# Performance work log

Measured on AMD Instinct MI355X. Metric: run time of the kernel, lower is better.

## Reference

```python
import jax, jax.numpy as jnp
import numpy as np

B, S, D = 2, 2048, 4096
N_HEADS, N_KV_HEADS = 32, 8
HEAD_DIM = D // N_HEADS  # 128
N_REP = N_HEADS // N_KV_HEADS
NEG_INF = -1e9  # finite stand-in for -inf additive causal mask


def apply_rotary_emb(x, freqs_cis):
    # x: [b, s, h, hd]; freqs_cis: [s, hd//2, 2] (cos, sin)
    b, s, h, hd = x.shape
    xr = x.reshape(b, s, h, hd // 2, 2)
    fc = freqs_cis.reshape(1, s, 1, hd // 2, 2)
    o0 = xr[..., 0] * fc[..., 0] - xr[..., 1] * fc[..., 1]
    o1 = xr[..., 1] * fc[..., 0] + xr[..., 0] * fc[..., 1]
    return jnp.stack([o0, o1], axis=-1).reshape(b, s, h, hd)


def setup_inputs() -> dict:
    key = jax.random.key(0)
    ks = jax.random.split(key, 6)
    x = jax.random.normal(ks[0], (B, S, D), dtype=jnp.float32)
    # weights stored torch-style: [out_features, in_features]
    wq = jax.random.normal(ks[1], (N_HEADS * HEAD_DIM, D), dtype=jnp.float32) * 0.02
    wk = jax.random.normal(ks[2], (N_KV_HEADS * HEAD_DIM, D), dtype=jnp.float32) * 0.02
    wv = jax.random.normal(ks[3], (N_KV_HEADS * HEAD_DIM, D), dtype=jnp.float32) * 0.02
    wo = jax.random.normal(ks[4], (D, N_HEADS * HEAD_DIM), dtype=jnp.float32) * 0.02
    # rotary table (Llama-style, theta=10000)
    inv_freq = 1.0 / (10000.0 ** (np.arange(0, HEAD_DIM, 2, dtype=np.float32) / HEAD_DIM))
    angles = np.arange(S, dtype=np.float32)[:, None] * inv_freq[None, :]
    freqs_cis = jnp.asarray(np.stack([np.cos(angles), np.sin(angles)], axis=-1))  # [S, hd//2, 2]
    # additive causal mask
    mask = jnp.where(jnp.tril(jnp.ones((S, S), dtype=bool)), 0.0, NEG_INF).astype(jnp.float32)
    return {"x": x, "start_pos": 0, "freqs_cis": freqs_cis, "mask": mask,
            "wq": wq, "wk": wk, "wv": wv, "wo": wo}


def reference(x, start_pos, freqs_cis, mask, wq, wk, wv, wo):
    b, s, _ = x.shape
    xq = jnp.einsum('bsd,ed->bse', x, wq).reshape(b, s, N_HEADS, HEAD_DIM)
    xk = jnp.einsum('bsd,ed->bse', x, wk).reshape(b, s, N_KV_HEADS, HEAD_DIM)
    xv = jnp.einsum('bsd,ed->bse', x, wv).reshape(b, s, N_KV_HEADS, HEAD_DIM)
    xq = apply_rotary_emb(xq, freqs_cis)
    xk = apply_rotary_emb(xk, freqs_cis)
    # repeat_kv (repeat_interleave along head dim)
    xk = jnp.repeat(xk, N_REP, axis=2)
    xv = jnp.repeat(xv, N_REP, axis=2)
    q = xq.transpose(0, 2, 1, 3)  # [b, h, s, hd]
    k = xk.transpose(0, 2, 1, 3)
    v = xv.transpose(0, 2, 1, 3)
    scores = jnp.einsum('bhqd,bhkd->bhqk', q, k) / jnp.sqrt(jnp.float32(HEAD_DIM))
    scores = scores + mask[None, None, :, :]
    probs = jax.nn.softmax(scores.astype(jnp.float32), axis=-1).astype(q.dtype)
    out = jnp.einsum('bhqk,bhkd->bhqd', probs, v)
    out = out.transpose(0, 2, 1, 3).reshape(b, s, N_HEADS * HEAD_DIM)
    return jnp.einsum('bse,de->bsd', out, wo)
```

## Files before the change

### kernel.cpp

```cpp
#include <hip/hip_runtime.h>
#include <cstdint>
#include <cstddef>

#define B_   2
#define S_   2048
#define D_   4096
#define H_   32
#define KVH_ 8
#define HD_  128

typedef unsigned short u16;
typedef short     bf16x8 __attribute__((ext_vector_type(8)));
typedef float     f32x4  __attribute__((ext_vector_type(4)));
typedef float     f32x16 __attribute__((ext_vector_type(16)));
typedef u16       u16x8  __attribute__((ext_vector_type(8)));
typedef uint32_t  u32x2  __attribute__((ext_vector_type(2)));
typedef uint32_t  u32x4  __attribute__((ext_vector_type(4)));

__device__ __forceinline__ u16 f2bf(float f) {
  union { float f; uint32_t u; } v; v.f = f;
  uint32_t u = v.u;
  return (u16)((u + 0x7fffu + ((u >> 16) & 1u)) >> 16);
}
__device__ __forceinline__ float bf2f(u16 h) {
  union { uint32_t u; float f; } v; v.u = ((uint32_t)h) << 16;
  return v.f;
}
__device__ __forceinline__ uint32_t cvtpk(float lo, float hi_) {
  uint32_t r; asm("v_cvt_pk_bf16_f32 %0, %1, %2" : "=v"(r) : "v"(lo), "v"(hi_)); return r;
}
__device__ __forceinline__ float exp2v(float x) {
  float r; asm("v_exp_f32 %0, %1" : "=v"(r) : "v"(x)); return r;
}

__device__ __forceinline__ void gl_lds16(const void* g, void* l) {
  __builtin_amdgcn_global_load_lds(
      (const __attribute__((address_space(1))) void*)g,
      (__attribute__((address_space(3))) void*)l, 16, 0, 0);
}

#define MFMA(a, b, c)  __builtin_amdgcn_mfma_f32_16x16x32_bf16((a), (b), (c), 0, 0, 0)
#define MFMA32(a, b, c) __builtin_amdgcn_mfma_f32_32x32x16_bf16((a), (b), (c), 0, 0, 0)
#define PLSWAP(x, y) asm volatile("v_permlane32_swap_b32 %0, %1" : "+v"(x), "+v"(y))

__global__ void cast_kernel(const float* __restrict__ in, u16* __restrict__ out, int n8) {
  int i = blockIdx.x * blockDim.x + threadIdx.x;
  if (i >= n8) return;
  const float4* p = (const float4*)in + (size_t)i * 2;
  float4 a = p[0], b = p[1];
  u16x8 r;
  r[0] = f2bf(a.x); r[1] = f2bf(a.y); r[2] = f2bf(a.z); r[3] = f2bf(a.w);
  r[4] = f2bf(b.x); r[5] = f2bf(b.y); r[6] = f2bf(b.z); r[7] = f2bf(b.w);
  *((u16x8*)out + i) = r;
}

template <bool OUT_F32>
__global__ __launch_bounds__(256, 2)
void gemm_bt(const u16* __restrict__ A, const u16* __restrict__ Bw,
             void* __restrict__ C, int M, int N, int K) {
  __shared__ u16 lA[128 * 32];
  __shared__ u16 lB[128 * 32];
  const int tid = threadIdx.x;
  const int w = tid >> 6, l = tid & 63;
  const int lc = l & 15, lg = l >> 4;
  const int bn = blockIdx.x, bm = blockIdx.y;
  const int wr = w >> 1, wc = w & 1;
  const u16* Ab = A + (size_t)(bm * 128) * K;
  const u16* Bb = Bw + (size_t)(bn * 128) * K;
  const int srow = l >> 2;
  const int scol = (l & 3) * 8;

  f32x4 acc[4][4];
#pragma unroll
  for (int i = 0; i < 4; ++i)
#pragma unroll
    for (int j = 0; j < 4; ++j) acc[i][j] = (f32x4){0.f, 0.f, 0.f, 0.f};

  const int nk = K >> 5;
  for (int kt = 0; kt < nk; ++kt) {
    const int k0 = kt * 32;
    __syncthreads();
#pragma unroll
    for (int i = 0; i < 2; ++i) {
      const int rowA = (w * 2 + i) * 16;
      gl_lds16(Ab + (size_t)(rowA + srow) * K + k0 + scol, &lA[rowA * 32]);
      gl_lds16(Bb + (size_t)(rowA + srow) * K + k0 + scol, &lB[rowA * 32]);
    }
    __syncthreads();
    bf16x8 af[4], bfr[4];
#pragma unroll
    for (int mi = 0; mi < 4; ++mi)
      af[mi] = *(const bf16x8*)&lA[(wr * 64 + mi * 16 + lc) * 32 + lg * 8];
#pragma unroll
    for (int ni = 0; ni < 4; ++ni)
      bfr[ni] = *(const bf16x8*)&lB[(wc * 64 + ni * 16 + lc) * 32 + lg * 8];
#pragma unroll
    for (int mi = 0; mi < 4; ++mi)
#pragma unroll
      for (int ni = 0; ni < 4; ++ni)
        acc[mi][ni] = MFMA(af[mi], bfr[ni], acc[mi][ni]);
  }

#pragma unroll
  for (int mi = 0; mi < 4; ++mi)
#pragma unroll
    for (int ni = 0; ni < 4; ++ni)
#pragma unroll
      for (int r = 0; r < 4; ++r) {
        const int row = bm * 128 + wr * 64 + mi * 16 + lg * 4 + r;
        const int col = bn * 128 + wc * 64 + ni * 16 + lc;
        if constexpr (OUT_F32)
          ((float*)C)[(size_t)row * N + col] = acc[mi][ni][r];
        else
          ((u16*)C)[(size_t)row * N + col] = f2bf(acc[mi][ni][r]);
      }
}

template <bool OUT_F32>
__global__ __launch_bounds__(512, 2)
void gemm256_bt(const u16* __restrict__ A, const u16* __restrict__ Bw,
                void* __restrict__ C, int M, int N, int K) {
  __shared__ u16 sA[2 * 256 * 64];
  __shared__ u16 sB[2 * 256 * 64];
  const int tid = threadIdx.x;
  const int w = tid >> 6, l = tid & 63;
  const int lc = l & 15, lg = l >> 4;
  const int wm = w >> 2, wn = w & 3;
  const int nbn = N >> 8;
  const int nwg = (M >> 8) * nbn;
  const int cpx = nwg >> 3;
  const int lin = blockIdx.x;
  const int swz = (lin & 7) * cpx + (lin >> 3);
  const int bm = swz / nbn, bn = swz % nbn;
  const u16* Ab = A + (size_t)(bm * 256) * K;
  const u16* Bb = Bw + (size_t)(bn * 256) * K;
  const int lr = l >> 3;
  const int scc = ((l & 7) ^ lr) * 8;
  int cxg[2];
#pragma unroll
  for (int kk = 0; kk < 2; ++kk) cxg[kk] = ((kk * 4 + lg) ^ (lc & 7)) * 8;

  f32x4 acc[8][4];
#pragma unroll
  for (int i = 0; i < 8; ++i)
#pragma unroll
    for (int j = 0; j < 4; ++j) acc[i][j] = (f32x4){0.f, 0.f, 0.f, 0.f};

  auto STAGEA = [&](int buf, int t1, int h) {
    const int k0 = t1 * 64;
#pragma unroll
    for (int j = 0; j < 2; ++j) {
      const int r0 = h * 128 + w * 16 + j * 8;
      gl_lds16(Ab + (size_t)(r0 + lr) * K + k0 + scc, &sA[buf * 16384 + r0 * 64]);
    }
  };
  auto STAGEB = [&](int buf, int t1, int h) {
    const int k0 = t1 * 64;
#pragma unroll
    for (int j = 0; j < 2; ++j) {
      const int r0 = h * 128 + w * 16 + j * 8;
      gl_lds16(Bb + (size_t)(r0 + lr) * K + k0 + scc, &sB[buf * 16384 + r0 * 64]);
    }
  };

  STAGEA(0, 0, 0); STAGEA(0, 0, 1);
  STAGEB(0, 0, 0); STAGEB(0, 0, 1);
  asm volatile("s_waitcnt vmcnt(0)" ::: "memory");
  __builtin_amdgcn_s_barrier();
  asm volatile("" ::: "memory");

  const int nk = K >> 6;
  for (int t = 0; t < nk; ++t) {
    const int cur = t & 1;
    const int cb = cur * 16384;
    const bool pf = (t + 1 < nk);
#pragma unroll
    for (int p = 0; p < 4; ++p) {
      const int qm = p >> 1, qn = p & 1;
      bf16x8 af[4][2], bfr[2][2];
#pragma unroll
      for (int mi = 0; mi < 4; ++mi)
#pragma unroll
        for (int kk = 0; kk < 2; ++kk)
          af[mi][kk] = *(const bf16x8*)
              &sA[cb + (wm * 128 + qm * 64 + mi * 16 + lc) * 64 + cxg[kk]];
#pragma unroll
      for (int ni = 0; ni < 2; ++ni)
#pragma unroll
        for (int kk = 0; kk < 2; ++kk)
          bfr[ni][kk] = *(const bf16x8*)
              &sB[cb + (wn * 64 + qn * 32 + ni * 16 + lc) * 64 + cxg[kk]];
      if (pf && p == 0) {
        STAGEA(cur ^ 1, t + 1, 0); STAGEA(cur ^ 1, t + 1, 1);
        STAGEB(cur ^ 1, t + 1, 0); STAGEB(cur ^ 1, t + 1, 1);
      }
      __builtin_amdgcn_s_barrier();
      asm volatile("s_waitcnt lgkmcnt(0)" ::: "memory");
      __builtin_amdgcn_sched_barrier(0);
      __builtin_amdgcn_s_setprio(1);
#pragma unroll
      for (int kk = 0; kk < 2; ++kk)
#pragma unroll
        for (int mi = 0; mi < 4; ++mi)
#pragma unroll
          for (int ni = 0; ni < 2; ++ni)
            acc[qm * 4 + mi][qn * 2 + ni] =
                MFMA(af[mi][kk], bfr[ni][kk], acc[qm * 4 + mi][qn * 2 + ni]);
      __builtin_amdgcn_s_setprio(0);
      if (p == 3) asm volatile("s_waitcnt vmcnt(0)" ::: "memory");
      __builtin_amdgcn_s_barrier();
      asm volatile("" ::: "memory");
    }
  }

#pragma unroll
  for (int mi = 0; mi < 8; ++mi)
#pragma unroll
    for (int ni = 0; ni < 4; ++ni)
#pragma unroll
      for (int r = 0; r < 4; ++r) {
        const int row = bm * 256 + wm * 128 + mi * 16 + lg * 4 + r;
        const int col = bn * 256 + wn * 64 + ni * 16 + lc;
        if constexpr (OUT_F32)
          ((float*)C)[(size_t)row * N + col] = acc[mi][ni][r];
        else
          ((u16*)C)[(size_t)row * N + col] = f2bf(acc[mi][ni][r]);
      }
}

template <int NH, int STRIDE, int OFF>
__global__ void rope_kernel(const u16* __restrict__ lin, const float* __restrict__ fr,
                            u16* __restrict__ out, float scale) {
  int idx = blockIdx.x * 256 + threadIdx.x;
  const int total = B_ * S_ * NH * 64;
  if (idx >= total) return;
  const int i = idx & 63;
  const int h = (idx >> 6) % NH;
  const int t = idx / (64 * NH);
  const int s = t & (S_ - 1);
  const int b = t >> 11;
  const size_t src = (size_t)t * STRIDE + OFF + h * HD_ + 2 * i;
  const float x0 = bf2f(lin[src]);
  const float x1 = bf2f(lin[src + 1]);
  const float2 cs = ((const float2*)fr)[s * 64 + i];
  const float o0 = (x0 * cs.x - x1 * cs.y) * scale;
  const float o1 = (x1 * cs.x + x0 * cs.y) * scale;
  const size_t dst = ((size_t)((b * NH + h) * S_ + s)) * HD_ + 2 * i;
  out[dst] = f2bf(o0);
  out[dst + 1] = f2bf(o1);
}

__global__ void vtrans_kernel(const u16* __restrict__ kvlin, u16* __restrict__ vt) {
  __shared__ u16 tile[32][33];
  const int tx = threadIdx.x, ty = threadIdx.y;
  const int s0 = blockIdx.x * 32;
  const int d0 = blockIdx.y * 32;
  const int bk = blockIdx.z;
  const int b = bk >> 3, kv = bk & 7;
#pragma unroll
  for (int r = 0; r < 4; ++r) {
    const int s = s0 + ty + r * 8;
    tile[ty + r * 8][tx] =
        kvlin[((size_t)(b * S_ + s)) * 2048 + 1024 + kv * HD_ + d0 + tx];
  }
  __syncthreads();
#pragma unroll
  for (int r = 0; r < 4; ++r) {
    const int d = d0 + ty + r * 8;
    vt[((size_t)bk * HD_ + d) * S_ + s0 + tx] = tile[tx][ty + r * 8];
  }
}

__global__ __launch_bounds__(256, 2)
void attn_kernel(const u16* __restrict__ Q, const u16* __restrict__ K,
                 const u16* __restrict__ V, u16* __restrict__ O) {
  __shared__ u16 sK[2][64 * HD_];
  __shared__ u16 sV[2][HD_ * 64];
  const int tid = threadIdx.x;
  const int w = tid >> 6, l = tid & 63;
  const int hi = l >> 5, q32 = l & 31;
  const int kv = blockIdx.y, b = blockIdx.z;
  const int h = kv * 4 + w;
  const u16* Kp = K + ((size_t)(b * KVH_ + kv) * S_) * HD_;
  const u16* Vp = V + ((size_t)(b * KVH_ + kv) * HD_) * S_;

  int koff[4], voff[4];
#pragma unroll
  for (int i = 0; i < 4; ++i) {
    const int kr = w * 16 + i * 4 + (l >> 4);
    koff[i] = kr * HD_ + (((l & 15) ^ (kr & 7))) * 8;
    const int vr = w * 32 + i * 8 + (l >> 3);
    voff[i] = vr * S_ + (((l & 7) ^ (vr & 7))) * 8;
  }
  int cx[8];
#pragma unroll
  for (int c = 0; c < 8; ++c) cx[c] = ((c * 2 + hi) ^ (l & 7)) * 8;

  auto STAGE = [&](int bufi, int ti) {
    const u16* kg = Kp + (size_t)ti * (64 * HD_);
    const u16* vg = Vp + (size_t)ti * 64;
#pragma unroll
    for (int i = 0; i < 4; ++i) {
      gl_lds16(kg + koff[i], &sK[bufi][(w * 16 + i * 4) * HD_]);
      gl_lds16(vg + voff[i], &sV[bufi][(w * 32 + i * 8) * 64]);
    }
  };

  int cur = 0;
  for (int seg = 0; seg < 2; ++seg) {
    const int qt = seg ? (63 - blockIdx.x) : blockIdx.x;
    const int qg = qt * 32 + q32;
    const u16* Qp = Q + ((size_t)(b * H_ + h) * S_ + qt * 32) * HD_;

    bf16x8 qf[8];
#pragma unroll
    for (int ds = 0; ds < 8; ++ds)
      qf[ds] = *(const bf16x8*)(Qp + (size_t)q32 * HD_ + ds * 16 + hi * 8);
    asm volatile("s_waitcnt vmcnt(0)" ::: "memory");

    f32x16 out[4];
#pragma unroll
    for (int d = 0; d < 4; ++d)
#pragma unroll
      for (int r = 0; r < 16; ++r) out[d][r] = 0.f;
    float mrun = -1e30f, lrun = 0.f;

    const int nt = (qt >> 1) + 1;
    STAGE(cur, 0);

    for (int t = 0; t < nt; ++t) {
      if (t + 1 < nt) {
        STAGE(cur ^ 1, t + 1);
        asm volatile("s_waitcnt vmcnt(8)" ::: "memory");
      } else {
        asm volatile("s_waitcnt vmcnt(0)" ::: "memory");
      }
      __builtin_amdgcn_s_barrier();
      asm volatile("" ::: "memory");

      f32x16 sc0, sc1;
#pragma unroll
      for (int r = 0; r < 16; ++r) { sc0[r] = 0.f; sc1[r] = 0.f; }
      __builtin_amdgcn_s_setprio(1);
#pragma unroll
      for (int ds = 0; ds < 8; ++ds) {
        bf16x8 kf0 = *(const bf16x8*)&sK[cur][q32 * HD_ + cx[ds]];
        bf16x8 kf1 = *(const bf16x8*)&sK[cur][(32 + q32) * HD_ + cx[ds]];
        sc0 = MFMA32(kf0, qf[ds], sc0);
        sc1 = MFMA32(kf1, qf[ds], sc1);
      }
      __builtin_amdgcn_s_setprio(0);

      const bool diag = (t == nt - 1);
      float p0[16], p1[16];
#pragma unroll
      for (int r = 0; r < 16; ++r) {
        const int krow = (r & 3) + 8 * (r >> 2) + 4 * hi;
        float v0 = sc0[r], v1 = sc1[r];
        if (diag) {
          if (t * 64 + krow > qg) v0 = -1e9f;
          if (t * 64 + 32 + krow > qg) v1 = -1e9f;
        }
        p0[r] = v0; p1[r] = v1;
      }
      float rm = -1e30f;
#pragma unroll
      for (int r = 0; r < 16; ++r) rm = fmaxf(rm, fmaxf(p0[r], p1[r]));
      rm = fmaxf(rm, __shfl_xor(rm, 32, 64));
      if (!__all(rm <= mrun + 8.0f)) {
        const float mnew = fmaxf(mrun, rm);
        const float alpha = exp2v(mrun - mnew);
        mrun = mnew;
        lrun *= alpha;
#pragma unroll
        for (int d = 0; d < 4; ++d) out[d] *= alpha;
      }
      float sum = 0.f;
#pragma unroll
      for (int r = 0; r < 16; ++r) {
        p0[r] = exp2v(p0[r] - mrun);
        p1[r] = exp2v(p1[r] - mrun);
        sum += p0[r] + p1[r];
      }
      sum += __shfl_xor(sum, 32, 64);
      lrun += sum;
      uint32_t pk0[8], pk1[8];
#pragma unroll
      for (int g = 0; g < 4; ++g) {
        pk0[2 * g]     = cvtpk(p0[4 * g], p0[4 * g + 1]);
        pk0[2 * g + 1] = cvtpk(p0[4 * g + 2], p0[4 * g + 3]);
        pk1[2 * g]     = cvtpk(p1[4 * g], p1[4 * g + 1]);
        pk1[2 * g + 1] = cvtpk(p1[4 * g + 2], p1[4 * g + 3]);
      }
      PLSWAP(pk0[0], pk0[2]); PLSWAP(pk0[1], pk0[3]);
      PLSWAP(pk0[4], pk0[6]); PLSWAP(pk0[5], pk0[7]);
      PLSWAP(pk1[0], pk1[2]); PLSWAP(pk1[1], pk1[3]);
      PLSWAP(pk1[4], pk1[6]); PLSWAP(pk1[5], pk1[7]);
      bf16x8 pa[4];
      pa[0] = __builtin_bit_cast(bf16x8, (u32x4){pk0[0], pk0[1], pk0[2], pk0[3]});
      pa[1] = __builtin_bit_cast(bf16x8, (u32x4){pk0[4], pk0[5], pk0[6], pk0[7]});
      pa[2] = __builtin_bit_cast(bf16x8, (u32x4){pk1[0], pk1[1], pk1[2], pk1[3]});
      pa[3] = __builtin_bit_cast(bf16x8, (u32x4){pk1[4], pk1[5], pk1[6], pk1[7]});
      __builtin_amdgcn_s_setprio(1);
#pragma unroll
      for (int d = 0; d < 4; ++d) {
        const int vbase = (d * 32 + q32) * 64;
#pragma unroll
        for (int kk = 0; kk < 4; ++kk) {
          bf16x8 vf = *(const bf16x8*)&sV[cur][vbase + cx[kk]];
          out[d] = MFMA32(vf, pa[kk], out[d]);
        }
      }
      __builtin_amdgcn_s_setprio(0);
      asm volatile("" ::: "memory");
      __builtin_amdgcn_s_barrier();
      cur ^= 1;
    }

    const float inv = 1.0f / lrun;
    u16* myS = ((u16*)sK) + w * 4096;
#pragma unroll
    for (int d = 0; d < 4; ++d)
#pragma unroll
      for (int rq = 0; rq < 4; ++rq) {
        u32x2 pw;
        pw[0] = cvtpk(out[d][rq * 4 + 0] * inv, out[d][rq * 4 + 1] * inv);
        pw[1] = cvtpk(out[d][rq * 4 + 2] * inv, out[d][rq * 4 + 3] * inv);
        const int gin = (d * 8 + rq * 2 + hi) ^ (q32 & 15);
        *(u32x2*)&myS[q32 * 128 + gin * 4] = pw;
      }
    asm volatile("s_waitcnt lgkmcnt(0)" ::: "memory");
    __builtin_amdgcn_sched_barrier(0);
    const int rr = l >> 4;
    const int cc = l & 15;
#pragma unroll
    for (int p = 0; p < 8; ++p) {
      const int q = p * 4 + rr;
      const int ga = (2 * cc) ^ (q & 15);
      const int gb = (2 * cc + 1) ^ (q & 15);
      u32x2 va = *(const u32x2*)&myS[q * 128 + ga * 4];
      u32x2 vb = *(const u32x2*)&myS[q * 128 + gb * 4];
      u32x4 val = {va[0], va[1], vb[0], vb[1]};
      *(u32x4*)&O[((size_t)(b * S_ + qt * 32 + q)) * (H_ * HD_) + h * HD_ + cc * 8] = val;
    }
    if (seg == 0) {
      asm volatile("" ::: "memory");
      __builtin_amdgcn_s_barrier();
    }
  }
}

extern "C" void kernel_launch(void* const* d_in, const int* in_sizes, int n_in,
                              void* d_out, int out_size, void* d_ws, size_t ws_size,
                              hipStream_t stream) {
  const float* x     = (const float*)d_in[0];
  const float* freqs = (const float*)d_in[2];
  const float* wq    = (const float*)d_in[4];
  const float* wk    = (const float*)d_in[5];
  const float* wv    = (const float*)d_in[6];
  const float* wo    = (const float*)d_in[7];

  char* ws = (char*)d_ws;
  u16* xb    = (u16*)(ws + 0);
  u16* wqb   = (u16*)(ws + 33554432);
  u16* wkb   = (u16*)(ws + 67108864);
  u16* wvb   = (u16*)(ws + 75497472);
  u16* qlin  = (u16*)(ws + 83886080);
  u16* kvlin = (u16*)(ws + 117440512);
  u16* qr   = wqb;
  u16* kr   = wkb;
  u16* vt   = wvb;
  u16* aout = qlin;
  u16* wob  = xb;

  cast_kernel<<<8192, 256, 0, stream>>>(x, xb, 2097152);
  cast_kernel<<<8192, 256, 0, stream>>>(wq, wqb, 2097152);
  cast_kernel<<<2048, 256, 0, stream>>>(wk, wkb, 524288);
  cast_kernel<<<2048, 256, 0, stream>>>(wv, wvb, 524288);
  gemm256_bt<false><<<256, 512, 0, stream>>>(xb, wqb, qlin, 4096, 4096, 4096);
  gemm_bt<false><<<dim3(16, 32), 256, 0, stream>>>(xb, wkb, kvlin, 4096, 2048, 4096);
  rope_kernel<32, 4096, 0><<<32768, 256, 0, stream>>>(qlin, freqs, qr,
      0.08838834764831845f * 1.4426950408889634f);
  rope_kernel<8, 2048, 0><<<8192, 256, 0, stream>>>(kvlin, freqs, kr, 1.0f);
  vtrans_kernel<<<dim3(64, 4, 16), dim3(32, 8), 0, stream>>>(kvlin, vt);
  attn_kernel<<<dim3(32, 8, 2), 256, 0, stream>>>(qr, kr, vt, aout);
  cast_kernel<<<8192, 256, 0, stream>>>(wo, wob, 2097152);
  gemm256_bt<true><<<256, 512, 0, stream>>>(aout, wob, d_out, 4096, 4096, 4096);
}
```

Before: 572.6 us.

## Stagger GEMM half-tile loads with fine-grained vmcnt waits and remap warp quadrants

Reworks the bf16 GEMM main loop so each 128-row half of the A and B tiles is loaded separately and at different sub-steps. Loads for the next tile and the tile after it are issued into both LDS buffers, with partial vmcnt waits so compute can start on a quadrant before the whole tile has arrived. Warp-to-quadrant mapping changes so each sub-step consumes exactly one A half and one B half, matching the staggered arrival order. One of the two barriers per sub-step is dropped. This hides global-load latency better, but the hand-counted vmcnt values must exactly match the number of outstanding loads, so a miscount risks races or wrong results.

```diff
diff --git a/kernel.cpp b/kernel.cpp
--- a/kernel.cpp
+++ b/kernel.cpp
@@ -163,38 +163,39 @@
     }
   };
 
-  STAGEA(0, 0, 0); STAGEA(0, 0, 1);
-  STAGEB(0, 0, 0); STAGEB(0, 0, 1);
-  asm volatile("s_waitcnt vmcnt(0)" ::: "memory");
-  __builtin_amdgcn_s_barrier();
-  asm volatile("" ::: "memory");
-
   const int nk = K >> 6;
+  STAGEA(0, 0, 0); STAGEB(0, 0, 0);
+  STAGEB(0, 0, 1); STAGEA(0, 0, 1);
+  if (nk > 1) { STAGEA(1, 1, 0); STAGEB(1, 1, 0); }
+
   for (int t = 0; t < nk; ++t) {
     const int cur = t & 1;
     const int cb = cur * 16384;
-    const bool pf = (t + 1 < nk);
+    const int nb = (cur ^ 1);
 #pragma unroll
     for (int p = 0; p < 4; ++p) {
-      const int qm = p >> 1, qn = p & 1;
+      const int ha = p >> 1, hb = p & 1;
+      if (p == 0)      asm volatile("s_waitcnt vmcnt(8)" ::: "memory");
+      else if (p == 1) asm volatile("s_waitcnt vmcnt(10)" ::: "memory");
+      else if (p == 2) asm volatile("s_waitcnt vmcnt(8)" ::: "memory");
+      __builtin_amdgcn_s_barrier();
+      asm volatile("" ::: "memory");
       bf16x8 af[4][2], bfr[2][2];
 #pragma unroll
       for (int mi = 0; mi < 4; ++mi)
 #pragma unroll
         for (int kk = 0; kk < 2; ++kk)
           af[mi][kk] = *(const bf16x8*)
-              &sA[cb + (wm * 128 + qm * 64 + mi * 16 + lc) * 64 + cxg[kk]];
+              &sA[cb + (ha * 128 + wm * 64 + mi * 16 + lc) * 64 + cxg[kk]];
 #pragma unroll
       for (int ni = 0; ni < 2; ++ni)
 #pragma unroll
         for (int kk = 0; kk < 2; ++kk)
           bfr[ni][kk] = *(const bf16x8*)
-              &sB[cb + (wn * 64 + qn * 32 + ni * 16 + lc) * 64 + cxg[kk]];
-      if (pf && p == 0) {
-        STAGEA(cur ^ 1, t + 1, 0); STAGEA(cur ^ 1, t + 1, 1);
-        STAGEB(cur ^ 1, t + 1, 0); STAGEB(cur ^ 1, t + 1, 1);
-      }
-      __builtin_amdgcn_s_barrier();
+              &sB[cb + (hb * 128 + wn * 32 + ni * 16 + lc) * 64 + cxg[kk]];
+      if (p == 0 && t + 1 < nk) { STAGEB(nb, t + 1, 1); STAGEA(nb, t + 1, 1); }
+      if (p == 2 && t + 2 < nk) { STAGEA(cur, t + 2, 0); }
+      if (p == 3 && t + 2 < nk) { STAGEB(cur, t + 2, 0); }
       asm volatile("s_waitcnt lgkmcnt(0)" ::: "memory");
       __builtin_amdgcn_sched_barrier(0);
       __builtin_amdgcn_s_setprio(1);
@@ -204,28 +205,29 @@
         for (int mi = 0; mi < 4; ++mi)
 #pragma unroll
           for (int ni = 0; ni < 2; ++ni)
-            acc[qm * 4 + mi][qn * 2 + ni] =
-                MFMA(af[mi][kk], bfr[ni][kk], acc[qm * 4 + mi][qn * 2 + ni]);
+            acc[ha * 4 + mi][hb * 2 + ni] =
+                MFMA(af[mi][kk], bfr[ni][kk], acc[ha * 4 + mi][hb * 2 + ni]);
       __builtin_amdgcn_s_setprio(0);
-      if (p == 3) asm volatile("s_waitcnt vmcnt(0)" ::: "memory");
-      __builtin_amdgcn_s_barrier();
-      asm volatile("" ::: "memory");
-    }
-  }
-
-#pragma unroll
-  for (int mi = 0; mi < 8; ++mi)
-#pragma unroll
-    for (int ni = 0; ni < 4; ++ni)
-#pragma unroll
-      for (int r = 0; r < 4; ++r) {
-        const int row = bm * 256 + wm * 128 + mi * 16 + lg * 4 + r;
-        const int col = bn * 256 + wn * 64 + ni * 16 + lc;
-        if constexpr (OUT_F32)
-          ((float*)C)[(size_t)row * N + col] = acc[mi][ni][r];
-        else
-          ((u16*)C)[(size_t)row * N + col] = f2bf(acc[mi][ni][r]);
-      }
+    }
+  }
+
+#pragma unroll
+  for (int ha = 0; ha < 2; ++ha)
+#pragma unroll
+    for (int mi = 0; mi < 4; ++mi)
+#pragma unroll
+      for (int hb = 0; hb < 2; ++hb)
+#pragma unroll
+        for (int ni = 0; ni < 2; ++ni)
+#pragma unroll
+          for (int r = 0; r < 4; ++r) {
+            const int row = bm * 256 + ha * 128 + wm * 64 + mi * 16 + lg * 4 + r;
+            const int col = bn * 256 + hb * 128 + wn * 32 + ni * 16 + lc;
+            if constexpr (OUT_F32)
+              ((float*)C)[(size_t)row * N + col] = acc[ha * 4 + mi][hb * 2 + ni][r];
+            else
+              ((u16*)C)[(size_t)row * N + col] = f2bf(acc[ha * 4 + mi][hb * 2 + ni][r]);
+          }
 }
 
 template <int NH, int STRIDE, int OFF>
```

Measured after the change: 527.1 us. 1.09x faster.
